# Performance work log

Hardware: AMD Instinct MI355X
Metric: run time of the kernel (lower is better)

Reference implementation:

```python
import jax, jax.numpy as jnp
from jax import lax
import numpy as np

# Config mirroring CSABlock(embed_dim=128, bs=8, heads=8, img_size=512, depth=2)
E = 128
BATCH = 8
HEADS = 8
RESO = 512 // 8      # 64
DEPTH = 2
SPLIT = 2            # split_size
C = 2 * E            # token dim = 256
C2 = C // 2          # per-branch dim
NH = HEADS // 2      # heads per branch
HID = 4 * C          # mlp hidden (mlp_ratio=4)
EPS = 1e-5


def setup_inputs() -> dict:
    key = jax.random.key(0)
    ks = iter(jax.random.split(key, 24))
    rn = lambda s, sd=0.02: jax.random.normal(next(ks), s, jnp.float32) * sd
    return {
        "x1": jax.random.normal(next(ks), (BATCH, E, RESO, RESO), jnp.float32),
        "x2": jax.random.normal(next(ks), (BATCH, E, RESO, RESO), jnp.float32),
        # conv_embed: Conv2d(C,C,3,1,1) + BatchNorm (eval) + LayerNorm
        "conv_w": rn((C, C, 3, 3)), "conv_b": jnp.zeros((C,), jnp.float32),
        "bn_g": jnp.ones((C,), jnp.float32), "bn_b": jnp.zeros((C,), jnp.float32),
        "bn_m": rn((C,), 0.1), "bn_v": jax.random.uniform(next(ks), (C,), jnp.float32) + 0.5,
        "ln0_g": jnp.ones((C,), jnp.float32), "ln0_b": jnp.zeros((C,), jnp.float32),
        # per-CSWinBlock params, stacked over DEPTH
        "n1_g": jnp.ones((DEPTH, C), jnp.float32), "n1_b": jnp.zeros((DEPTH, C), jnp.float32),
        "qkv_w": rn((DEPTH, C, 3 * C)),                       # Linear(dim, 3*dim, bias=False)
        "lepe_w": rn((DEPTH, 2, C2, 1, 3, 3)),                # depthwise get_v conv per branch
        "lepe_b": jnp.zeros((DEPTH, 2, C2), jnp.float32),
        "proj_w": rn((DEPTH, C, C)), "proj_b": jnp.zeros((DEPTH, C), jnp.float32),
        "n2_g": jnp.ones((DEPTH, C), jnp.float32), "n2_b": jnp.zeros((DEPTH, C), jnp.float32),
        "fc1_w": rn((DEPTH, C, HID)), "fc1_b": jnp.zeros((DEPTH, HID), jnp.float32),
        "fc2_w": rn((DEPTH, HID, C)), "fc2_b": jnp.zeros((DEPTH, C), jnp.float32),
    }


def _ln(x, g, b):
    mu = jnp.mean(x, -1, keepdims=True)
    var = jnp.mean((x - mu) ** 2, -1, keepdims=True)
    return (x - mu) * lax.rsqrt(var + EPS) * g + b


def _branch(q, k, v, Hs, Ws, dw_w, dw_b):
    """LePEAttention: cross-shaped stripe window attention with locally-enhanced PE.
    q,k,v: (B, L, C2); stripes of size Hs x Ws over a RESO x RESO grid."""
    B, L, c2 = q.shape
    H = W = RESO
    hd = c2 // NH
    scale = hd ** -0.5

    def to_win(t):  # (B,L,c2) -> (B*nW, NH, Hs*Ws, hd)
        t = t.reshape(B, H // Hs, Hs, W // Ws, Ws, c2)
        t = t.transpose(0, 1, 3, 2, 4, 5).reshape(-1, Hs * Ws, NH, hd)
        return t.transpose(0, 2, 1, 3)

    qw, kw = to_win(q), to_win(k)
    # v as per-window images for the depthwise LePE conv (padding is per-window)
    vimg = v.reshape(B, H // Hs, Hs, W // Ws, Ws, c2).transpose(0, 1, 3, 5, 2, 4)
    vimg = vimg.reshape(-1, c2, Hs, Ws)
    lepe = lax.conv_general_dilated(vimg, dw_w, (1, 1), [(1, 1), (1, 1)],
                                    dimension_numbers=("NCHW", "OIHW", "NCHW"),
                                    feature_group_count=c2) + dw_b[:, None, None]
    heads = lambda t: t.reshape(-1, NH, hd, Hs * Ws).transpose(0, 1, 3, 2)
    vw, lepe = heads(vimg), heads(lepe)

    attn = jax.nn.softmax(jnp.einsum("wnsd,wntd->wnst", qw * scale, kw), axis=-1)
    o = jnp.einsum("wnst,wntd->wnsd", attn, vw) + lepe      # (B*nW, NH, S, hd)
    # windows2img
    o = o.transpose(0, 2, 1, 3).reshape(B, H // Hs, W // Ws, Hs, Ws, c2)
    o = o.transpose(0, 1, 3, 2, 4, 5).reshape(B, L, c2)
    return o


def _forward(x1, x2, conv_w, conv_b, bn_g, bn_b, bn_m, bn_v, ln0_g, ln0_b,
             n1_g, n1_b, qkv_w, lepe_w, lepe_b, proj_w, proj_b,
             n2_g, n2_b, fc1_w, fc1_b, fc2_w, fc2_b):
    B, _, H, W = x1.shape
    t = jnp.concatenate([x1, x2], 1)                                   # (B, C, H, W)
    t = lax.conv_general_dilated(t, conv_w, (1, 1), [(1, 1), (1, 1)],
                                 dimension_numbers=("NCHW", "OIHW", "NCHW")) + conv_b[:, None, None]
    # BatchNorm2d in eval mode (running stats)
    t = (t - bn_m[:, None, None]) * lax.rsqrt(bn_v + EPS)[:, None, None] * bn_g[:, None, None] + bn_b[:, None, None]
    t = t.reshape(B, C, H * W).transpose(0, 2, 1)                      # b c h w -> b (h w) c
    t = _ln(t, ln0_g, ln0_b)

    for i in range(DEPTH):  # CSWinBlock x DEPTH
        img = _ln(t, n1_g[i], n1_b[i])
        qkv = (img @ qkv_w[i]).reshape(B, -1, 3, C)
        q, k, v = qkv[..., 0, :], qkv[..., 1, :], qkv[..., 2, :]
        # branch 0: horizontal stripes (H_sp=RESO, W_sp=SPLIT); branch 1: vertical
        xa = _branch(q[..., :C2], k[..., :C2], v[..., :C2], RESO, SPLIT, lepe_w[i, 0], lepe_b[i, 0])
        xb = _branch(q[..., C2:], k[..., C2:], v[..., C2:], SPLIT, RESO, lepe_w[i, 1], lepe_b[i, 1])
        att = jnp.concatenate([xa, xb], -1) @ proj_w[i] + proj_b[i]
        t = t + att
        y = _ln(t, n2_g[i], n2_b[i])
        t = t + (jax.nn.gelu(y @ fc1_w[i] + fc1_b[i], approximate=False) @ fc2_w[i] + fc2_b[i])

    x = t.transpose(0, 2, 1).reshape(B, C, H, W)
    return x[:, :E], x[:, E:]


def reference(x1, x2, conv_w, conv_b, bn_g, bn_b, bn_m, bn_v, ln0_g, ln0_b,
              n1_g, n1_b, qkv_w, lepe_w, lepe_b, proj_w, proj_b,
              n2_g, n2_b, fc1_w, fc1_b, fc2_w, fc2_b):
    return _forward(x1, x2, conv_w, conv_b, bn_g, bn_b, bn_m, bn_v, ln0_g, ln0_b,
                    n1_g, n1_b, qkv_w, lepe_w, lepe_b, proj_w, proj_b,
                    n2_g, n2_b, fc1_w, fc1_b, fc2_w, fc2_b)
```

## Files before the change

### kernel.cpp

```cpp
#include <hip/hip_runtime.h>
#include <hip/hip_bf16.h>

#define EPSV 1e-5f

using s8v = __attribute__((ext_vector_type(8))) short;
using f4v = __attribute__((ext_vector_type(4))) float;

__device__ __forceinline__ float bf2f(ushort u){
  union { unsigned int i; float f; } x; x.i = ((unsigned int)u)<<16; return x.f;
}
__device__ __forceinline__ ushort f2bf(float f){
  union { float f; unsigned int i; } x; x.f = f;
  unsigned int r = x.i + 0x7FFFu + ((x.i>>16)&1u);
  return (ushort)(r>>16);
}
__device__ __forceinline__ float wsum(float s){
  #pragma unroll
  for (int m=1;m<64;m<<=1) s += __shfl_xor(s, m);
  return s;
}

__device__ __forceinline__ void gload16(const void* g, void* l){
  __builtin_amdgcn_global_load_lds((__attribute__((address_space(1))) void*)g,
                                   (__attribute__((address_space(3))) void*)l, 16, 0, 0);
}

__global__ __launch_bounds__(256) void repack_in_k(const float* __restrict__ x1,
                                                   const float* __restrict__ x2,
                                                   ushort* __restrict__ Xin){
  __shared__ ushort tile[256][66];
  const int y = blockIdx.x, b = blockIdx.y, tid = threadIdx.x;
  const int xl = tid & 63, cq = tid >> 6;
  for (int it=0; it<64; it++){
    int ci = it*4 + cq;
    float v;
    if (ci < 128) v = x1[(((long)b*128 + ci)*64 + y)*64 + xl];
    else          v = x2[(((long)b*128 + (ci-128))*64 + y)*64 + xl];
    tile[ci][xl] = f2bf(v);
  }
  __syncthreads();
  for (int x=0; x<64; x++){
    Xin[(((long)b*66 + (y+1))*66 + (x+1))*256 + tid] = tile[tid][x];
  }
}

__global__ void repack_convw_k(const float* __restrict__ w, ushort* __restrict__ Wc){
  const long total = 256L*2304;
  for (long e = (long)blockIdx.x*blockDim.x + threadIdx.x; e < total; e += (long)gridDim.x*blockDim.x){
    int co = (int)(e / 2304), kk = (int)(e % 2304);
    int dd = kk >> 8, ci = kk & 255;
    Wc[e] = f2bf(w[((long)(co*256 + ci))*9 + dd]);
  }
}

__global__ void transpose_w_k(const float* __restrict__ src, ushort* __restrict__ dst, int K, int N){
  long total = (long)K*N;
  for (long e = (long)blockIdx.x*blockDim.x + threadIdx.x; e < total; e += (long)gridDim.x*blockDim.x){
    int k = (int)(e / N), n = (int)(e % N);
    dst[(long)n*K + k] = f2bf(src[e]);
  }
}

__global__ void bnprep_k(const float* cb, const float* g, const float* b,
                         const float* m, const float* v, float* sc, float* sh){
  int n = threadIdx.x;
  if (n < 256){
    float s = g[n] * rsqrtf(v[n] + EPSV);
    sc[n] = s;
    sh[n] = (cb[n] - m[n])*s + b[n];
  }
}

template<int EPI>
__global__ __launch_bounds__(256) void gemm_f(
    const ushort* __restrict__ A, const ushort* __restrict__ Xin,
    const ushort* __restrict__ Wt, const float* __restrict__ bias,
    const float* __restrict__ sc, const float* __restrict__ sh,
    float* __restrict__ T, const float* __restrict__ g1, const float* __restrict__ b1,
    const float* __restrict__ g2, const float* __restrict__ b2,
    ushort* __restrict__ Xb, float* __restrict__ dout, int K)
{
  constexpr bool CONVA = (EPI==0);
  __shared__ ushort SMEM[32768];
  ushort* As = SMEM;
  ushort* Bs = SMEM + 4096;
  const int tid = threadIdx.x, wid = tid>>6, lane = tid&63;
  const int m0 = blockIdx.x*64;
  const int l15 = lane&15, lg = lane>>4;
  const int rS = wid*8 + (lane>>3);
  const int cA = (lane&7)*8;

  const ushort* pA[2];
  if (CONVA){
    #pragma unroll
    for (int j=0;j<2;j++){
      int t = m0 + j*32 + rS;
      int b = t>>12, y = (t>>6)&63, x = t&63;
      pA[j] = Xin + ((long)((b*66 + y+1)*66) + (x+1))*256 + cA;
    }
  } else {
    #pragma unroll
    for (int j=0;j<2;j++) pA[j] = A + (long)(m0 + j*32 + rS)*K + cA;
  }
  const ushort* pB[8];
  #pragma unroll
  for (int j=0;j<8;j++) pB[j] = Wt + (long)(j*32 + rS)*K + cA;

  f4v acc[4][4] = {};

  for (int k0=0; k0<K; k0+=64){
    int koffA;
    if (CONVA){
      int dd = k0 >> 8;
      int dy = dd/3, dx = dd - dy*3;
      koffA = ((dy-1)*66 + (dx-1))*256 + (k0 & 255);
    } else koffA = k0;
    #pragma unroll
    for (int j=0;j<2;j++)
      gload16(pA[j] + koffA, (void*)&As[(j*256 + wid*64)*8]);
    #pragma unroll
    for (int j=0;j<8;j++)
      gload16(pB[j] + k0, (void*)&Bs[(j*256 + wid*64)*8]);
    __syncthreads();
    #pragma unroll
    for (int kk=0; kk<2; kk++){
      s8v a[4], b[4];
      const int ke = kk*32 + lg*8;
      #pragma unroll
      for (int mi=0;mi<4;mi++) a[mi] = *(const s8v*)&As[(mi*16 + l15)*64 + ke];
      #pragma unroll
      for (int ni=0;ni<4;ni++) b[ni] = *(const s8v*)&Bs[(wid*64 + ni*16 + l15)*64 + ke];
      #pragma unroll
      for (int mi=0;mi<4;mi++)
        #pragma unroll
        for (int ni=0;ni<4;ni++)
          acc[mi][ni] = __builtin_amdgcn_mfma_f32_16x16x32_bf16(a[mi], b[ni], acc[mi][ni], 0,0,0);
    }
    __syncthreads();
  }

  float* CT = (float*)SMEM;
  #pragma unroll
  for (int mi=0;mi<4;mi++)
    #pragma unroll
    for (int ni=0;ni<4;ni++)
      #pragma unroll
      for (int r=0;r<4;r++)
        CT[(mi*16 + lg*4 + r)*256 + wid*64 + ni*16 + l15] = acc[mi][ni][r];
  __syncthreads();

  const int c0 = lane*4;
  float4 scv4, shv4, bias4, g1v, b1v, g2v, b2v;
  if (EPI==0){
    scv4 = *(const float4*)&sc[c0]; shv4 = *(const float4*)&sh[c0];
    g1v = *(const float4*)&g1[c0];  b1v = *(const float4*)&b1[c0];
    g2v = *(const float4*)&g2[c0];  b2v = *(const float4*)&b2[c0];
  } else {
    bias4 = *(const float4*)&bias[c0];
    if (EPI==1){ g1v = *(const float4*)&g1[c0]; b1v = *(const float4*)&b1[c0]; }
  }

  for (int t=0; t<16; t++){
    const int r = wid*16 + t;
    const long gmr = m0 + r;
    float4 v = *(float4*)&CT[r*256 + c0];
    float4 t4;
    if (EPI==0){
      t4.x = v.x*scv4.x + shv4.x; t4.y = v.y*scv4.y + shv4.y;
      t4.z = v.z*scv4.z + shv4.z; t4.w = v.w*scv4.w + shv4.w;
    } else {
      float4 rv = *(float4*)&T[gmr*256 + c0];
      t4.x = rv.x + v.x + bias4.x; t4.y = rv.y + v.y + bias4.y;
      t4.z = rv.z + v.z + bias4.z; t4.w = rv.w + v.w + bias4.w;
    }
    if (EPI==3){
      *(float4*)&CT[r*256 + c0] = t4;
    } else {
      float mu = wsum(t4.x+t4.y+t4.z+t4.w) * (1.0f/256.0f);
      float d0=t4.x-mu, d1=t4.y-mu, d2=t4.z-mu, d3=t4.w-mu;
      float rs = rsqrtf(wsum(d0*d0+d1*d1+d2*d2+d3*d3)*(1.0f/256.0f) + EPSV);
      if (EPI==0){
        float u0 = d0*rs*g1v.x + b1v.x, u1 = d1*rs*g1v.y + b1v.y;
        float u2 = d2*rs*g1v.z + b1v.z, u3 = d3*rs*g1v.w + b1v.w;
        float4 u = {u0,u1,u2,u3};
        *(float4*)&T[gmr*256 + c0] = u;
        float mu2 = wsum(u0+u1+u2+u3) * (1.0f/256.0f);
        float e0=u0-mu2, e1=u1-mu2, e2=u2-mu2, e3=u3-mu2;
        float rs2 = rsqrtf(wsum(e0*e0+e1*e1+e2*e2+e3*e3)*(1.0f/256.0f) + EPSV);
        ushort4 o; o.x=f2bf(e0*rs2*g2v.x + b2v.x); o.y=f2bf(e1*rs2*g2v.y + b2v.y);
        o.z=f2bf(e2*rs2*g2v.z + b2v.z); o.w=f2bf(e3*rs2*g2v.w + b2v.w);
        *(ushort4*)&Xb[gmr*256 + c0] = o;
      } else {
        *(float4*)&T[gmr*256 + c0] = t4;
        ushort4 o; o.x=f2bf(d0*rs*g1v.x + b1v.x); o.y=f2bf(d1*rs*g1v.y + b1v.y);
        o.z=f2bf(d2*rs*g1v.z + b1v.z); o.w=f2bf(d3*rs*g1v.w + b1v.w);
        *(ushort4*)&Xb[gmr*256 + c0] = o;
      }
    }
  }

  if (EPI==3){
    __syncthreads();
    const int b_ = m0>>12, y_ = (m0>>6)&63;
    float* obase = dout + (long)b_*524288 + (long)y_*64;
    for (int it=0; it<64; it++){
      int e = it*256 + tid;
      int c = e>>6, x = e&63;
      obase[(long)(c>>7)*4194304 + (long)(c&127)*4096 + x] = CT[x*256 + c];
    }
  }
}

#define BM 128
#define BN 128
#define BK 64
template<int EPI>
__global__ __launch_bounds__(256) void gemm_k(
    const ushort* __restrict__ A,
    const ushort* __restrict__ Wt, const float* __restrict__ bias,
    ushort* __restrict__ outb, int N, int K)
{
  __shared__ ushort SMEM[BM*BK + BN*BK];
  ushort* As = SMEM;
  ushort* Bs = SMEM + BM*BK;
  const int tid = threadIdx.x, wid = tid>>6, lane = tid&63;
  const int m0 = blockIdx.x*BM, n0 = blockIdx.y*BN;
  const int wm = (wid>>1)*64, wn = (wid&1)*64;
  const int l15 = lane&15, lg = lane>>4;

  const int rA = wid*32 + (lane>>3);
  const int cA = (lane&7)*8;
  const ushort* pA[4];
  #pragma unroll
  for (int j=0;j<4;j++) pA[j] = A + (long)(m0 + rA + j*8)*K + cA;
  const ushort* pB[4];
  #pragma unroll
  for (int j=0;j<4;j++) pB[j] = Wt + (long)(n0 + rA + j*8)*K + cA;

  f4v acc[4][4] = {};

  for (int k0=0; k0<K; k0+=BK){
    #pragma unroll
    for (int j=0;j<4;j++){
      gload16(pA[j] + k0, (void*)&As[(wid*32 + j*8)*BK]);
      gload16(pB[j] + k0, (void*)&Bs[(wid*32 + j*8)*BK]);
    }
    __syncthreads();
    #pragma unroll
    for (int kk=0; kk<2; kk++){
      s8v a[4], b[4];
      const int ke = kk*32 + lg*8;
      #pragma unroll
      for (int mi=0;mi<4;mi++) a[mi] = *(const s8v*)&As[(wm + mi*16 + l15)*BK + ke];
      #pragma unroll
      for (int ni=0;ni<4;ni++) b[ni] = *(const s8v*)&Bs[(wn + ni*16 + l15)*BK + ke];
      #pragma unroll
      for (int mi=0;mi<4;mi++)
        #pragma unroll
        for (int ni=0;ni<4;ni++)
          acc[mi][ni] = __builtin_amdgcn_mfma_f32_16x16x32_bf16(a[mi], b[ni], acc[mi][ni], 0,0,0);
    }
    __syncthreads();
  }

  if (EPI == 4){
    #pragma unroll
    for (int mi=0;mi<4;mi++)
      #pragma unroll
      for (int ni=0;ni<4;ni++)
        #pragma unroll
        for (int r=0;r<4;r++){
          int gm = m0 + wm + mi*16 + lg*4 + r;
          int gn = n0 + wn + ni*16 + l15;
          float v = acc[mi][ni][r];
          int tile = gn >> 8;
          int c = gn & 255;
          int br2 = (c >> 7) & 1;
          int hh = (c >> 5) & 3;
          int d = c & 31;
          int bb2 = gm >> 12;
          int y = (gm >> 6) & 63;
          int x = gm & 63;
          int wv, sv;
          if (br2 == 0){ wv = x >> 1; sv = (y << 1) | (x & 1); }
          else         { wv = y >> 1; sv = ((y & 1) << 6) | x; }
          long row = ((long)bb2*32 + wv)*128 + sv;
          outb[(((long)(tile*2 + br2)*4 + hh)*32768L + row)*32 + d] = f2bf(v);
        }
  } else {
    float* CT = (float*)SMEM;
    #pragma unroll
    for (int p=0; p<2; p++){
      if ((wid>>1) == p){
        #pragma unroll
        for (int mi=0;mi<4;mi++)
          #pragma unroll
          for (int ni=0;ni<4;ni++)
            #pragma unroll
            for (int r=0;r<4;r++)
              CT[(mi*16 + lg*4 + r)*128 + wn + ni*16 + l15] = acc[mi][ni][r];
      }
      __syncthreads();
      #pragma unroll
      for (int it=0; it<8; it++){
        int e = it*256 + tid;
        int row = e >> 5;
        int c4 = e & 31;
        float4 v = *(float4*)&CT[row*128 + c4*4];
        int gm = m0 + p*64 + row;
        int gn = n0 + c4*4;
        float4 bv = *(const float4*)&bias[gn];
        float t0 = v.x + bv.x, t1 = v.y + bv.y, t2 = v.z + bv.z, t3 = v.w + bv.w;
        t0 = 0.5f*t0*(1.0f + erff(t0*0.70710678118654752f));
        t1 = 0.5f*t1*(1.0f + erff(t1*0.70710678118654752f));
        t2 = 0.5f*t2*(1.0f + erff(t2*0.70710678118654752f));
        t3 = 0.5f*t3*(1.0f + erff(t3*0.70710678118654752f));
        ushort4 u; u.x=f2bf(t0); u.y=f2bf(t1); u.z=f2bf(t2); u.w=f2bf(t3);
        *(ushort4*)&outb[(long)gm*N + gn] = u;
      }
      __syncthreads();
    }
  }
}

template<int BR>
__global__ __launch_bounds__(256) void attn_k(
    const ushort* __restrict__ QKVw, ushort* __restrict__ ATT,
    const float* __restrict__ lepe_w, const float* __restrict__ lepe_b, int layer)
{
  __shared__ ushort q_lds[128][36];
  __shared__ ushort k_lds[128][36];
  __shared__ ushort vT[32][132];
  __shared__ float wl[32][9];
  __shared__ float bl[32];
  const int tid = threadIdx.x, wid = tid>>6, lane = tid&63;
  const int b = blockIdx.y;
  const int w = blockIdx.x>>2, h = blockIdx.x&3;
  const int choff = BR*128 + h*32;
  const int l15 = lane&15, lg = lane>>4;

  const long rowbase = ((long)b*32 + w)*128;
  const ushort* qb = QKVw + (((long)(0*2+BR)*4 + h)*32768L + rowbase)*32;
  const ushort* kb = QKVw + (((long)(1*2+BR)*4 + h)*32768L + rowbase)*32;
  const ushort* vb = QKVw + (((long)(2*2+BR)*4 + h)*32768L + rowbase)*32;

  for (int e = tid; e < 512; e += 256){
    int row = e>>2, c4 = (e&3)*8;
    *(uint4*)&q_lds[row][c4] = *(const uint4*)(qb + (long)e*8);
    *(uint4*)&k_lds[row][c4] = *(const uint4*)(kb + (long)e*8);
    uint4 val = *(const uint4*)(vb + (long)e*8);
    const ushort* u = (const ushort*)&val;
    #pragma unroll
    for (int jj=0;jj<8;jj++) vT[c4+jj][row] = u[jj];
  }
  for (int e = tid; e < 288; e += 256){
    int d = e/9, tap = e%9;
    wl[d][tap] = lepe_w[((long)((layer*2+BR)*128 + h*32 + d))*9 + tap];
  }
  if (tid < 32) bl[tid] = lepe_b[(layer*2+BR)*128 + h*32 + tid];
  __syncthreads();

  const int wrow = wid*32;
  const float scale = 0.17677669529663689f;
  const int srcE = (lane & 15) | ((lane & 16) << 1);
  const int srcO = srcE + 16;
  const bool hi = (lane >= 32);

  #pragma unroll
  for (int mi=0; mi<2; mi++){
    s8v aq = *(const s8v*)&q_lds[wrow + mi*16 + l15][lg*8];
    f4v S[8];
    #pragma unroll
    for (int ni=0; ni<8; ni++){
      s8v bk = *(const s8v*)&k_lds[ni*16 + l15][lg*8];
      f4v z = {0.f,0.f,0.f,0.f};
      S[ni] = __builtin_amdgcn_mfma_f32_16x16x32_bf16(bk, aq, z, 0,0,0);
    }
    float mx = -1e30f;
    #pragma unroll
    for (int ni=0; ni<8; ni++)
      #pragma unroll
      for (int r=0;r<4;r++){ S[ni][r] *= scale; mx = fmaxf(mx, S[ni][r]); }
    mx = fmaxf(mx, __shfl_xor(mx, 16));
    mx = fmaxf(mx, __shfl_xor(mx, 32));
    float sum = 0.f;
    #pragma unroll
    for (int ni=0; ni<8; ni++)
      #pragma unroll
      for (int r=0;r<4;r++){ S[ni][r] = __expf(S[ni][r]-mx); sum += S[ni][r]; }
    sum += __shfl_xor(sum, 16);
    sum += __shfl_xor(sum, 32);
    const float inv = 1.0f / sum;
    unsigned int Alo[8], Ahi[8];
    #pragma unroll
    for (int ni=0; ni<8; ni++){
      Alo[ni] = (unsigned)f2bf(S[ni][0]*inv) | ((unsigned)f2bf(S[ni][1]*inv)<<16);
      Ahi[ni] = (unsigned)f2bf(S[ni][2]*inv) | ((unsigned)f2bf(S[ni][3]*inv)<<16);
    }
    f4v acc2[2] = {{0.f,0.f,0.f,0.f},{0.f,0.f,0.f,0.f}};
    #pragma unroll
    for (int ks=0; ks<4; ks++){
      unsigned e0 = (unsigned)__shfl((int)Alo[2*ks],   srcE);
      unsigned e1 = (unsigned)__shfl((int)Ahi[2*ks],   srcE);
      unsigned e2 = (unsigned)__shfl((int)Alo[2*ks+1], srcE);
      unsigned e3 = (unsigned)__shfl((int)Ahi[2*ks+1], srcE);
      unsigned o0 = (unsigned)__shfl((int)Alo[2*ks],   srcO);
      unsigned o1 = (unsigned)__shfl((int)Ahi[2*ks],   srcO);
      unsigned o2 = (unsigned)__shfl((int)Alo[2*ks+1], srcO);
      unsigned o3 = (unsigned)__shfl((int)Ahi[2*ks+1], srcO);
      union { unsigned u[4]; s8v v; } ap;
      ap.u[0] = hi?e2:e0; ap.u[1] = hi?e3:e1; ap.u[2] = hi?o2:o0; ap.u[3] = hi?o3:o1;
      #pragma unroll
      for (int di=0; di<2; di++){
        s8v bv = *(const s8v*)&vT[di*16 + l15][ks*32 + lg*8];
        acc2[di] = __builtin_amdgcn_mfma_f32_16x16x32_bf16(ap.v, bv, acc2[di], 0,0,0);
      }
    }
    #pragma unroll
    for (int di=0; di<2; di++)
      #pragma unroll
      for (int r=0;r<4;r++){
        int s = wrow + mi*16 + lg*4 + r;
        int d = di*16 + l15;
        float v = acc2[di][r] + bl[d];
        const int HsL = (BR==0)?64:2, WsL = (BR==0)?2:64;
        int hs, ws2;
        if (BR==0){ hs = s>>1; ws2 = s&1; }
        else      { hs = s>>6; ws2 = s&63; }
        #pragma unroll
        for (int a=-1;a<=1;a++)
          #pragma unroll
          for (int bb=-1;bb<=1;bb++){
            int h2 = hs+a, w2 = ws2+bb;
            if (h2>=0 && h2<HsL && w2>=0 && w2<WsL){
              int s2 = h2*WsL + w2;
              v += wl[d][(a+1)*3 + (bb+1)] * bf2f(vT[d][s2]);
            }
          }
        int y, x;
        if (BR==0){ y = s>>1; x = (w<<1)|(s&1); }
        else      { y = (w<<1)|(s>>6); x = s&63; }
        long tok = ((long)b*64 + y)*64 + x;
        ATT[tok*256 + choff + d] = f2bf(v);
      }
  }
}

extern "C" void kernel_launch(void* const* d_in, const int* in_sizes, int n_in,
                              void* d_out, int out_size, void* d_ws, size_t ws_size,
                              hipStream_t stream)
{
  (void)in_sizes; (void)n_in; (void)out_size;
  const float* x1     = (const float*)d_in[0];
  const float* x2     = (const float*)d_in[1];
  const float* conv_w = (const float*)d_in[2];
  const float* conv_b = (const float*)d_in[3];
  const float* bn_g   = (const float*)d_in[4];
  const float* bn_b   = (const float*)d_in[5];
  const float* bn_m   = (const float*)d_in[6];
  const float* bn_v   = (const float*)d_in[7];
  const float* ln0_g  = (const float*)d_in[8];
  const float* ln0_b  = (const float*)d_in[9];
  const float* n1_g   = (const float*)d_in[10];
  const float* n1_b   = (const float*)d_in[11];
  const float* qkv_w  = (const float*)d_in[12];
  const float* lepe_w = (const float*)d_in[13];
  const float* lepe_b = (const float*)d_in[14];
  const float* proj_w = (const float*)d_in[15];
  const float* proj_b = (const float*)d_in[16];
  const float* n2_g   = (const float*)d_in[17];
  const float* n2_b   = (const float*)d_in[18];
  const float* fc1_w  = (const float*)d_in[19];
  const float* fc1_b  = (const float*)d_in[20];
  const float* fc2_w  = (const float*)d_in[21];
  const float* fc2_b  = (const float*)d_in[22];

  if (ws_size < 121767936ULL){
    hipMemsetAsync(d_out, 0, (size_t)out_size*4, stream);
    return;
  }

  char* ws = (char*)d_ws;
  ushort* Xin  = (ushort*)ws;
  ushort* QKVb = (ushort*)ws;
  ushort* H1b  = (ushort*)ws;
  ushort* ATTb = (ushort*)(ws + 50331648);
  float*  T    = (float*)(ws + 67108864);
  ushort* Xb   = (ushort*)(ws + 100663296);
  size_t off = 117440512;
  ushort* Wc   = (ushort*)(ws + off); off += 1179648;
  ushort* Wq   = (ushort*)(ws + off); off += 786432;
  ushort* Wp   = (ushort*)(ws + off); off += 262144;
  ushort* W1   = (ushort*)(ws + off); off += 1048576;
  ushort* W2   = (ushort*)(ws + off); off += 1048576;
  float*  scv  = (float*)(ws + off);  off += 1024;
  float*  shv  = (float*)(ws + off);  off += 1024;

  hipMemsetAsync(Xin, 0, (size_t)8*66*66*256*2, stream);
  repack_in_k<<<dim3(64,8), 256, 0, stream>>>(x1, x2, Xin);
  repack_convw_k<<<576, 256, 0, stream>>>(conv_w, Wc);
  for (int i=0;i<2;i++){
    transpose_w_k<<<512,256,0,stream>>>(qkv_w + (long)i*196608, Wq + (long)i*196608, 256, 768);
    transpose_w_k<<<128,256,0,stream>>>(proj_w + (long)i*65536, Wp + (long)i*65536, 256, 256);
    transpose_w_k<<<512,256,0,stream>>>(fc1_w + (long)i*262144, W1 + (long)i*262144, 256, 1024);
    transpose_w_k<<<512,256,0,stream>>>(fc2_w + (long)i*262144, W2 + (long)i*262144, 1024, 256);
  }
  bnprep_k<<<1,256,0,stream>>>(conv_b, bn_g, bn_b, bn_m, bn_v, scv, shv);

  gemm_f<0><<<512,256,0,stream>>>(nullptr, Xin, Wc, nullptr, scv, shv,
                                  T, ln0_g, ln0_b, n1_g, n1_b, Xb, nullptr, 2304);

  for (int i=0;i<2;i++){
    gemm_k<4><<<dim3(256,6),256,0,stream>>>(Xb, Wq + (long)i*196608, nullptr, QKVb, 768, 256);
    attn_k<0><<<dim3(128,8),256,0,stream>>>(QKVb, ATTb, lepe_w, lepe_b, i);
    attn_k<1><<<dim3(128,8),256,0,stream>>>(QKVb, ATTb, lepe_w, lepe_b, i);
    gemm_f<1><<<512,256,0,stream>>>(ATTb, nullptr, Wp + (long)i*65536, proj_b + i*256,
                                    nullptr, nullptr, T, n2_g + i*256, n2_b + i*256,
                                    nullptr, nullptr, Xb, nullptr, 256);
    gemm_k<1><<<dim3(256,8),256,0,stream>>>(Xb, W1 + (long)i*262144, fc1_b + i*1024, H1b, 1024, 256);
    if (i == 0){
      gemm_f<1><<<512,256,0,stream>>>(H1b, nullptr, W2, fc2_b,
                                      nullptr, nullptr, T, n1_g + 256, n1_b + 256,
                                      nullptr, nullptr, Xb, nullptr, 1024);
    } else {
      gemm_f<3><<<512,256,0,stream>>>(H1b, nullptr, W2 + 262144, fc2_b + 256,
                                      nullptr, nullptr, T, nullptr, nullptr,
                                      nullptr, nullptr, nullptr, (float*)d_out, 1024);
    }
  }
}
```

Baseline: 511.4 us.

## Double-buffer LDS in gemm_f and XOR-swizzle LDS layout in both GEMMs

gemm_f now uses two LDS buffers, so the global-to-LDS load of the next K tile is issued while the current tile is multiplied, and one barrier per iteration is dropped. Both gemm_f and gemm_k apply an XOR swizzle to the 16-byte column chunks on the global-load side and the MFMA read side, to avoid LDS bank conflicts on the row-strided reads. gemm_f's shared memory grows to 80 KB per block, which may reduce occupancy.

```diff
diff --git a/kernel.cpp b/kernel.cpp
--- a/kernel.cpp
+++ b/kernel.cpp
@@ -81,14 +81,12 @@
     ushort* __restrict__ Xb, float* __restrict__ dout, int K)
 {
   constexpr bool CONVA = (EPI==0);
-  __shared__ ushort SMEM[32768];
-  ushort* As = SMEM;
-  ushort* Bs = SMEM + 4096;
+  __shared__ ushort SMEM[40960];
   const int tid = threadIdx.x, wid = tid>>6, lane = tid&63;
   const int m0 = blockIdx.x*64;
   const int l15 = lane&15, lg = lane>>4;
   const int rS = wid*8 + (lane>>3);
-  const int cA = (lane&7)*8;
+  const int cS = (((lane&7) ^ (lane>>3))*8);
 
   const ushort* pA[2];
   if (CONVA){
@@ -96,19 +94,19 @@
     for (int j=0;j<2;j++){
       int t = m0 + j*32 + rS;
       int b = t>>12, y = (t>>6)&63, x = t&63;
-      pA[j] = Xin + ((long)((b*66 + y+1)*66) + (x+1))*256 + cA;
+      pA[j] = Xin + ((long)((b*66 + y+1)*66) + (x+1))*256 + cS;
     }
   } else {
     #pragma unroll
-    for (int j=0;j<2;j++) pA[j] = A + (long)(m0 + j*32 + rS)*K + cA;
+    for (int j=0;j<2;j++) pA[j] = A + (long)(m0 + j*32 + rS)*K + cS;
   }
   const ushort* pB[8];
   #pragma unroll
-  for (int j=0;j<8;j++) pB[j] = Wt + (long)(j*32 + rS)*K + cA;
-
-  f4v acc[4][4] = {};
-
-  for (int k0=0; k0<K; k0+=64){
+  for (int j=0;j<8;j++) pB[j] = Wt + (long)(j*32 + rS)*K + cS;
+
+  auto stage = [&](int buf, int k0){
+    ushort* AsB = SMEM + buf*20480;
+    ushort* BsB = AsB + 4096;
     int koffA;
     if (CONVA){
       int dd = k0 >> 8;
@@ -117,19 +115,29 @@
     } else koffA = k0;
     #pragma unroll
     for (int j=0;j<2;j++)
-      gload16(pA[j] + koffA, (void*)&As[(j*256 + wid*64)*8]);
+      gload16(pA[j] + koffA, (void*)&AsB[(j*256 + wid*64)*8]);
     #pragma unroll
     for (int j=0;j<8;j++)
-      gload16(pB[j] + k0, (void*)&Bs[(j*256 + wid*64)*8]);
-    __syncthreads();
+      gload16(pB[j] + k0, (void*)&BsB[(j*256 + wid*64)*8]);
+  };
+
+  f4v acc[4][4] = {};
+
+  int cur = 0;
+  stage(0, 0);
+  __syncthreads();
+  for (int k0=0; k0<K; k0+=64){
+    if (k0 + 64 < K) stage(cur^1, k0 + 64);
+    const ushort* AsB = SMEM + cur*20480;
+    const ushort* BsB = AsB + 4096;
     #pragma unroll
     for (int kk=0; kk<2; kk++){
       s8v a[4], b[4];
-      const int ke = kk*32 + lg*8;
-      #pragma unroll
-      for (int mi=0;mi<4;mi++) a[mi] = *(const s8v*)&As[(mi*16 + l15)*64 + ke];
-      #pragma unroll
-      for (int ni=0;ni<4;ni++) b[ni] = *(const s8v*)&Bs[(wid*64 + ni*16 + l15)*64 + ke];
+      const int kch = ((kk*4 + lg) ^ (l15 & 7))*8;
+      #pragma unroll
+      for (int mi=0;mi<4;mi++) a[mi] = *(const s8v*)&AsB[(mi*16 + l15)*64 + kch];
+      #pragma unroll
+      for (int ni=0;ni<4;ni++) b[ni] = *(const s8v*)&BsB[(wid*64 + ni*16 + l15)*64 + kch];
       #pragma unroll
       for (int mi=0;mi<4;mi++)
         #pragma unroll
@@ -137,6 +145,7 @@
           acc[mi][ni] = __builtin_amdgcn_mfma_f32_16x16x32_bf16(a[mi], b[ni], acc[mi][ni], 0,0,0);
     }
     __syncthreads();
+    cur ^= 1;
   }
 
   float* CT = (float*)SMEM;
@@ -229,13 +238,13 @@
   const int l15 = lane&15, lg = lane>>4;
 
   const int rA = wid*32 + (lane>>3);
-  const int cA = (lane&7)*8;
+  const int cS = (((lane&7) ^ (lane>>3))*8);
   const ushort* pA[4];
   #pragma unroll
-  for (int j=0;j<4;j++) pA[j] = A + (long)(m0 + rA + j*8)*K + cA;
+  for (int j=0;j<4;j++) pA[j] = A + (long)(m0 + rA + j*8)*K + cS;
   const ushort* pB[4];
   #pragma unroll
-  for (int j=0;j<4;j++) pB[j] = Wt + (long)(n0 + rA + j*8)*K + cA;
+  for (int j=0;j<4;j++) pB[j] = Wt + (long)(n0 + rA + j*8)*K + cS;
 
   f4v acc[4][4] = {};
 
@@ -249,11 +258,11 @@
     #pragma unroll
     for (int kk=0; kk<2; kk++){
       s8v a[4], b[4];
-      const int ke = kk*32 + lg*8;
-      #pragma unroll
-      for (int mi=0;mi<4;mi++) a[mi] = *(const s8v*)&As[(wm + mi*16 + l15)*BK + ke];
-      #pragma unroll
-      for (int ni=0;ni<4;ni++) b[ni] = *(const s8v*)&Bs[(wn + ni*16 + l15)*BK + ke];
+      const int kch = ((kk*4 + lg) ^ (l15 & 7))*8;
+      #pragma unroll
+      for (int mi=0;mi<4;mi++) a[mi] = *(const s8v*)&As[(wm + mi*16 + l15)*BK + kch];
+      #pragma unroll
+      for (int ni=0;ni<4;ni++) b[ni] = *(const s8v*)&Bs[(wn + ni*16 + l15)*BK + kch];
       #pragma unroll
       for (int mi=0;mi<4;mi++)
         #pragma unroll
```

Measured after the change: 486.5 us. 4.9% less time.
